# Performance work log

Hardware: AMD Instinct MI355X
Metric: run time of the kernel (lower is better)

Reference implementation:

```python
import jax, jax.numpy as jnp
import numpy as np

N = 50000
E = 800000
IN = 128
HID = 32
OUT = 32
H1, H2 = 4, 4
NEG_SLOPE = 0.2


def setup_inputs() -> dict:
    key = jax.random.key(0)
    ks = jax.random.split(key, 12)
    x = jax.random.normal(ks[0], (N, IN), dtype=jnp.float32)
    src = jax.random.randint(ks[1], (E,), 0, N, dtype=jnp.int32)
    dst = jax.random.randint(ks[2], (E,), 0, N, dtype=jnp.int32)
    s = 0.1
    # layer 1: fc (IN -> H1*HID, no bias), attn vectors (H1, HID), bias (H1*HID,)
    W1 = jax.random.normal(ks[3], (IN, H1 * HID), dtype=jnp.float32) * s
    al1 = jax.random.normal(ks[4], (H1, HID), dtype=jnp.float32) * s
    ar1 = jax.random.normal(ks[5], (H1, HID), dtype=jnp.float32) * s
    b1 = jnp.zeros((H1 * HID,), dtype=jnp.float32)
    # layer 2: fc (H1*HID -> H2*OUT, no bias)
    W2 = jax.random.normal(ks[6], (H1 * HID, H2 * OUT), dtype=jnp.float32) * s
    al2 = jax.random.normal(ks[7], (H2, OUT), dtype=jnp.float32) * s
    ar2 = jax.random.normal(ks[8], (H2, OUT), dtype=jnp.float32) * s
    b2 = jnp.zeros((H2 * OUT,), dtype=jnp.float32)
    return {"x": x, "W1": W1, "al1": al1, "ar1": ar1, "b1": b1,
            "W2": W2, "al2": al2, "ar2": ar2, "b2": b2,
            "src": src, "dst": dst}


def _gat_layer(x, W, al, ar, b, src, dst, n, h, d):
    # feat_drop is identity (eval mode)
    feat = (x @ W).reshape(n, h, d)                       # [N,H,D]
    el = jnp.einsum('nhd,hd->nh', feat, al)               # [N,H]
    er = jnp.einsum('nhd,hd->nh', feat, ar)               # [N,H]
    e = jax.nn.leaky_relu(el[src] + er[dst], NEG_SLOPE)   # [E,H] SDDMM
    # edge softmax over incoming edges of each destination node
    emax = jax.ops.segment_max(e, dst, num_segments=n)    # [N,H]
    emax = jnp.where(jnp.isfinite(emax), emax, 0.0)       # guard 0-in-degree
    w = jnp.exp(e - emax[dst])                            # [E,H]
    denom = jax.ops.segment_sum(w, dst, num_segments=n)   # [N,H]
    alpha = w / jnp.maximum(denom[dst], 1e-9)             # [E,H]; attn_drop identity
    # SpMM aggregation
    rst = jax.ops.segment_sum(feat[src] * alpha[:, :, None], dst, num_segments=n)
    # residual: in_feats == h*d for both layers -> DGL uses Identity res_fc
    rst = rst + x.reshape(n, h, d)
    rst = rst + b.reshape(1, h, d)
    return rst


def reference(x, W1, al1, ar1, b1, W2, al2, ar2, b2, src, dst):
    h = _gat_layer(x, W1, al1, ar1, b1, src, dst, N, H1, HID)
    h = jax.nn.elu(h)                                     # layer-1 activation
    h = h.reshape(N, H1 * HID)                            # flatten(1)
    h = _gat_layer(h, W2, al2, ar2, b2, src, dst, N, H2, OUT)
    return h.mean(axis=1)                                 # [N,OUT]
```

## Files before the change

kernel.cpp:

```cpp
#include <hip/hip_runtime.h>
#include <cstdint>
#include <cstddef>

#define NEG_SLOPE 0.2f

typedef __bf16 bf16x8 __attribute__((ext_vector_type(8)));
typedef float  f32x4  __attribute__((ext_vector_type(4)));

__device__ inline unsigned int bf16pair(float a, float b) {
    unsigned int ua = __float_as_uint(a), ub = __float_as_uint(b);
    ua += 0x7fffu + ((ua >> 16) & 1u);
    ub += 0x7fffu + ((ub >> 16) & 1u);
    return (ua >> 16) | (ub & 0xffff0000u);
}
__device__ inline unsigned short bf16r(float x) {
    unsigned int u = __float_as_uint(x);
    u += 0x7fffu + ((u >> 16) & 1u);
    return (unsigned short)(u >> 16);
}

__global__ __launch_bounds__(256) void wtrans_kernel(
    const float* __restrict__ W1, const float* __restrict__ W2,
    unsigned short* __restrict__ Wt1, unsigned short* __restrict__ Wt2)
{
    __shared__ float tile[64][65];
    const float* W = (blockIdx.x < 4) ? W1 : W2;
    unsigned short* Wt = (blockIdx.x < 4) ? Wt1 : Wt2;
    const int tb = blockIdx.x & 3;
    const int k0 = (tb >> 1) * 64, n0 = (tb & 1) * 64;
    const int c = threadIdx.x & 63, r4 = threadIdx.x >> 6;
#pragma unroll
    for (int i = 0; i < 16; ++i) {
        const int r = i * 4 + r4;
        tile[r][c] = W[(size_t)(k0 + r) * 128 + n0 + c];
    }
    __syncthreads();
#pragma unroll
    for (int i = 0; i < 16; ++i) {
        const int nn = i * 4 + r4;
        Wt[(size_t)(n0 + nn) * 128 + k0 + c] = bf16r(tile[c][nn]);
    }
}

__global__ __launch_bounds__(256, 3) void gemm_attn_kernel(
    const float* __restrict__ X, const unsigned short* __restrict__ Wt,
    const float* __restrict__ al, const float* __restrict__ ar,
    unsigned short* __restrict__ feat16, float* __restrict__ el,
    float* __restrict__ er, int n)
{
    __shared__ unsigned short sX[64][136];
    __shared__ unsigned short sW[128][136];

    const int t = threadIdx.x;
    const int rowbase = blockIdx.x * 64;

#pragma unroll
    for (int i = 0; i < 8; ++i) {
        const int idx = t + 256 * i;
        const int row = idx >> 5;
        const int kq  = (idx & 31) * 4;
        int g = rowbase + row; if (g >= n) g = n - 1;
        const float4 v = *(const float4*)&X[(size_t)g * 128 + kq];
        uint2 pk;
        pk.x = bf16pair(v.x, v.y);
        pk.y = bf16pair(v.z, v.w);
        *(uint2*)&sX[row][kq] = pk;
    }
#pragma unroll
    for (int i = 0; i < 8; ++i) {
        const int idx = t + 256 * i;
        const int row = idx >> 4;
        const int q   = idx & 15;
        *(uint4*)&sW[row][q * 8] = *(const uint4*)&Wt[(size_t)row * 128 + q * 8];
    }
    __syncthreads();

    const int lane = t & 63;
    const int w    = t >> 6;
    const int m    = lane & 15;
    const int g4   = lane >> 4;

    bf16x8 a[4];
#pragma unroll
    for (int ks = 0; ks < 4; ++ks)
        a[ks] = *(const bf16x8*)&sX[w * 16 + m][ks * 32 + g4 * 8];

    float elacc[4][4] = {{0}}, eracc[4][4] = {{0}};
    unsigned short fout[8][4];

#pragma unroll
    for (int ct = 0; ct < 8; ct += 2) {
        f32x4 acc0 = {0.f, 0.f, 0.f, 0.f}, acc1 = {0.f, 0.f, 0.f, 0.f};
        const int n0 = ct * 16 + m, n1 = n0 + 16;
#pragma unroll
        for (int ks = 0; ks < 4; ++ks) {
            const bf16x8 b0 = *(const bf16x8*)&sW[n0][ks * 32 + g4 * 8];
            const bf16x8 b1 = *(const bf16x8*)&sW[n1][ks * 32 + g4 * 8];
            acc0 = __builtin_amdgcn_mfma_f32_16x16x32_bf16(a[ks], b0, acc0, 0, 0, 0);
            acc1 = __builtin_amdgcn_mfma_f32_16x16x32_bf16(a[ks], b1, acc1, 0, 0, 0);
        }
        const int h = ct >> 1;
        const float al0 = al[n0], ar0 = ar[n0];
        const float al1 = al[n1], ar1 = ar[n1];
#pragma unroll
        for (int r = 0; r < 4; ++r) {
            elacc[r][h] += acc0[r] * al0 + acc1[r] * al1;
            eracc[r][h] += acc0[r] * ar0 + acc1[r] * ar1;
            fout[ct][r]     = bf16r(acc0[r]);
            fout[ct + 1][r] = bf16r(acc1[r]);
        }
    }

    __syncthreads();
#pragma unroll
    for (int ct = 0; ct < 8; ++ct)
#pragma unroll
        for (int r = 0; r < 4; ++r)
            sX[w * 16 + g4 * 4 + r][(ct & 1) * 16 + (ct >> 1) * 32 + m] = fout[ct][r];
    __syncthreads();
    {
        const int row = t >> 2;
        const int q   = t & 3;
        const int g   = rowbase + row;
        if (g < n) {
#pragma unroll
            for (int i = 0; i < 4; ++i) {
                const int c0 = q * 8 + i * 32;
                *(uint4*)&feat16[(size_t)g * 128 + c0] = *(const uint4*)&sX[row][c0];
            }
        }
    }

#pragma unroll
    for (int r = 0; r < 4; ++r)
#pragma unroll
        for (int h = 0; h < 4; ++h) {
            float a_ = elacc[r][h], b_ = eracc[r][h];
            a_ += __shfl_xor(a_, 1); b_ += __shfl_xor(b_, 1);
            a_ += __shfl_xor(a_, 2); b_ += __shfl_xor(b_, 2);
            a_ += __shfl_xor(a_, 4); b_ += __shfl_xor(b_, 4);
            a_ += __shfl_xor(a_, 8); b_ += __shfl_xor(b_, 8);
            elacc[r][h] = a_; eracc[r][h] = b_;
        }
    if (m == 0) {
#pragma unroll
        for (int r = 0; r < 4; ++r) {
            const int row = rowbase + w * 16 + g4 * 4 + r;
            if (row < n) {
#pragma unroll
                for (int h = 0; h < 4; ++h) {
                    el[(size_t)row * 4 + h] = elacc[r][h];
                    er[(size_t)row * 4 + h] = eracc[r][h];
                }
            }
        }
    }
}


__global__ void rank_kernel(const int* __restrict__ dst, int* __restrict__ deg,
                            int* __restrict__ rank, int E)
{
    const int e4 = (blockIdx.x * blockDim.x + threadIdx.x) * 4;
    if (e4 + 4 <= E) {
        const int4 d = *(const int4*)&dst[e4];
        int4 r;
        r.x = atomicAdd(&deg[d.x], 1);
        r.y = atomicAdd(&deg[d.y], 1);
        r.z = atomicAdd(&deg[d.z], 1);
        r.w = atomicAdd(&deg[d.w], 1);
        *(int4*)&rank[e4] = r;
    } else {
        for (int e = e4; e < E; ++e) rank[e] = atomicAdd(&deg[dst[e]], 1);
    }
}

__global__ __launch_bounds__(1024) void scan_kernel(
    const int* __restrict__ deg, int* __restrict__ off, int n)
{
    __shared__ int wsums[16];
    __shared__ int s_carry;
    const int tid  = threadIdx.x;
    const int lane = tid & 63;
    const int wid  = tid >> 6;

    if (tid == 0) { s_carry = 0; off[0] = 0; }
    __syncthreads();

    const int n4 = n >> 2;
    const int4* __restrict__ deg4 = (const int4*)deg;

    for (int base = 0; base < n4; base += 1024) {
        const int i4 = base + tid;
        int4 v = make_int4(0, 0, 0, 0);
        if (i4 < n4) v = deg4[i4];
        const int t0 = v.x, t1 = t0 + v.y, t2 = t1 + v.z, t3 = t2 + v.w;

        int x = t3;
#pragma unroll
        for (int d = 1; d < 64; d <<= 1) {
            int y = __shfl_up(x, d);
            if (lane >= d) x += y;
        }
        if (lane == 63) wsums[wid] = x;
        __syncthreads();

        if (wid == 0 && lane < 16) {
            int xx = wsums[lane];
#pragma unroll
            for (int d = 1; d < 16; d <<= 1) {
                int y = __shfl_up(xx, d);
                if (lane >= d) xx += y;
            }
            wsums[lane] = xx;
        }
        __syncthreads();

        const int wp   = (wid == 0) ? 0 : wsums[wid - 1];
        const int excl = s_carry + wp + (x - t3);
        if (i4 < n4) {
            off[4 * i4 + 1] = excl + t0;
            off[4 * i4 + 2] = excl + t1;
            off[4 * i4 + 3] = excl + t2;
            off[4 * i4 + 4] = excl + t3;
        }
        __syncthreads();
        if (tid == 0) s_carry += wsums[15];
        __syncthreads();
    }
}

__global__ void place_kernel(const int* __restrict__ src, const int* __restrict__ dst,
                             const int* __restrict__ off, const int* __restrict__ rank,
                             int* __restrict__ csr_src, int E)
{
    const int e4 = (blockIdx.x * blockDim.x + threadIdx.x) * 4;
    if (e4 + 4 <= E) {
        const int4 s = *(const int4*)&src[e4];
        const int4 d = *(const int4*)&dst[e4];
        const int4 r = *(const int4*)&rank[e4];
        const int o0 = off[d.x], o1 = off[d.y], o2 = off[d.z], o3 = off[d.w];
        csr_src[o0 + r.x] = s.x;
        csr_src[o1 + r.y] = s.y;
        csr_src[o2 + r.z] = s.z;
        csr_src[o3 + r.w] = s.w;
    } else {
        for (int e = e4; e < E; ++e)
            csr_src[off[dst[e]] + rank[e]] = src[e];
    }
}

template <bool LAYER2>
__global__ __launch_bounds__(256) void agg_kernel(
    const int* __restrict__ off, const int* __restrict__ csr_src,
    const unsigned short* __restrict__ feat16, const float* __restrict__ el,
    const float* __restrict__ er, const float* __restrict__ resid,
    const float* __restrict__ bias, float* __restrict__ out, int n)
{
    const int lane = threadIdx.x & 63;
    const int node = blockIdx.x * 4 + (threadIdx.x >> 6);
    if (node >= n) return;

    const int h  = lane >> 4;
    const int d0 = 2 * lane;

    const float erh = er[(size_t)node * 4 + h];
    const unsigned int* __restrict__ fb = (const unsigned int*)feat16;

    const int beg = off[node], end = off[node + 1];

    float acc0 = 0.f, acc1 = 0.f, sw = 0.f;
    int j = beg;

#define EDGE4(J)                                                              \
    {                                                                         \
        const int s0 = csr_src[J], s1 = csr_src[(J) + 1];                     \
        const int s2 = csr_src[(J) + 2], s3 = csr_src[(J) + 3];               \
        const float e0 = el[(size_t)s0 * 4 + h];                              \
        const float e1 = el[(size_t)s1 * 4 + h];                              \
        const float e2 = el[(size_t)s2 * 4 + h];                              \
        const float e3 = el[(size_t)s3 * 4 + h];                              \
        const unsigned int u0 = fb[(size_t)s0 * 64 + lane];                   \
        const unsigned int u1 = fb[(size_t)s1 * 64 + lane];                   \
        const unsigned int u2 = fb[(size_t)s2 * 64 + lane];                   \
        const unsigned int u3 = fb[(size_t)s3 * 64 + lane];                   \
        float a0 = e0 + erh, a1 = e1 + erh, a2 = e2 + erh, a3 = e3 + erh;     \
        a0 = (a0 >= 0.f) ? a0 : NEG_SLOPE * a0;                               \
        a1 = (a1 >= 0.f) ? a1 : NEG_SLOPE * a1;                               \
        a2 = (a2 >= 0.f) ? a2 : NEG_SLOPE * a2;                               \
        a3 = (a3 >= 0.f) ? a3 : NEG_SLOPE * a3;                               \
        const float w0 = __expf(a0), w1 = __expf(a1);                         \
        const float w2 = __expf(a2), w3 = __expf(a3);                         \
        acc0 += w0 * __uint_as_float(u0 << 16);                               \
        acc1 += w0 * __uint_as_float(u0 & 0xffff0000u);                       \
        acc0 += w1 * __uint_as_float(u1 << 16);                               \
        acc1 += w1 * __uint_as_float(u1 & 0xffff0000u);                       \
        acc0 += w2 * __uint_as_float(u2 << 16);                               \
        acc1 += w2 * __uint_as_float(u2 & 0xffff0000u);                       \
        acc0 += w3 * __uint_as_float(u3 << 16);                               \
        acc1 += w3 * __uint_as_float(u3 & 0xffff0000u);                       \
        sw += w0 + w1 + w2 + w3;                                              \
    }

    for (; j + 8 <= end; j += 8) { EDGE4(j) EDGE4(j + 4) }
    for (; j + 4 <= end; j += 4) { EDGE4(j) }
#undef EDGE4
    for (; j < end; ++j) {
        const int s = csr_src[j];
        float e = el[(size_t)s * 4 + h] + erh;
        e = (e >= 0.f) ? e : NEG_SLOPE * e;
        const float w = __expf(e);
        const unsigned int u = fb[(size_t)s * 64 + lane];
        acc0 += w * __uint_as_float(u << 16);
        acc1 += w * __uint_as_float(u & 0xffff0000u);
        sw += w;
    }

    const float inv = 1.f / fmaxf(sw, 1e-9f);
    const float2 rs = *(const float2*)&resid[(size_t)node * 128 + d0];
    float v0 = acc0 * inv + rs.x + bias[d0];
    float v1 = acc1 * inv + rs.y + bias[d0 + 1];

    if (!LAYER2) {
        v0 = (v0 > 0.f) ? v0 : expm1f(v0);
        v1 = (v1 > 0.f) ? v1 : expm1f(v1);
        *(float2*)&out[(size_t)node * 128 + d0] = make_float2(v0, v1);
    } else {
        float s0 = v0, s1 = v1;
        s0 += __shfl_xor(s0, 16); s1 += __shfl_xor(s1, 16);
        s0 += __shfl_xor(s0, 32); s1 += __shfl_xor(s1, 32);
        if (lane < 16)
            *(float2*)&out[(size_t)node * 32 + 2 * lane] =
                make_float2(s0 * 0.25f, s1 * 0.25f);
    }
}

extern "C" void kernel_launch(void* const* d_in, const int* in_sizes, int n_in,
                              void* d_out, int out_size, void* d_ws, size_t ws_size,
                              hipStream_t stream)
{
    const float* x   = (const float*)d_in[0];
    const float* W1  = (const float*)d_in[1];
    const float* al1 = (const float*)d_in[2];
    const float* ar1 = (const float*)d_in[3];
    const float* b1  = (const float*)d_in[4];
    const float* W2  = (const float*)d_in[5];
    const float* al2 = (const float*)d_in[6];
    const float* ar2 = (const float*)d_in[7];
    const float* b2  = (const float*)d_in[8];
    const int*   src = (const int*)d_in[9];
    const int*   dst = (const int*)d_in[10];

    const int n = in_sizes[0] / 128;
    const int E = in_sizes[9];
    float* out = (float*)d_out;

    char* p = (char*)d_ws;
    float* h1    = (float*)p;          p += (size_t)n * 128 * sizeof(float);
    unsigned short* feat16 = (unsigned short*)p; p += (size_t)n * 128 * sizeof(unsigned short);
    float* el    = (float*)p;          p += (size_t)n * 4 * sizeof(float);
    float* er    = (float*)p;          p += (size_t)n * 4 * sizeof(float);
    int* off     = (int*)p;            p += (size_t)(n + 1) * sizeof(int);
    int* deg     = (int*)p;            p += (size_t)n * sizeof(int);
    int* rank    = (int*)p;            p += (size_t)E * sizeof(int);
    int* csr     = (int*)p;            p += (size_t)E * sizeof(int);
    unsigned short* wt1 = (unsigned short*)p; p += (size_t)128 * 128 * sizeof(unsigned short);
    unsigned short* wt2 = (unsigned short*)p; p += (size_t)128 * 128 * sizeof(unsigned short);

    hipMemsetAsync(deg, 0, (size_t)n * sizeof(int), stream);

    const int gemm_grid  = (n + 63) / 64;
    const int edge4_grid = (E / 4 + 255) / 256;
    const int agg_grid   = (n + 3) / 4;

    wtrans_kernel<<<8, 256, 0, stream>>>(W1, W2, wt1, wt2);
    gemm_attn_kernel<<<gemm_grid, 256, 0, stream>>>(x, wt1, al1, ar1, feat16, el, er, n);
    rank_kernel<<<edge4_grid, 256, 0, stream>>>(dst, deg, rank, E);
    scan_kernel<<<1, 1024, 0, stream>>>(deg, off, n);
    place_kernel<<<edge4_grid, 256, 0, stream>>>(src, dst, off, rank, csr, E);
    agg_kernel<false><<<agg_grid, 256, 0, stream>>>(off, csr, feat16, el, er, x, b1, h1, n);
    gemm_attn_kernel<<<gemm_grid, 256, 0, stream>>>(h1, wt2, al2, ar2, feat16, el, er, n);
    agg_kernel<true><<<agg_grid, 256, 0, stream>>>(off, csr, feat16, el, er, h1, b2, out, n);
}
```

Baseline: 271.4 us.

## Split wavefront into two half-waves processing alternate edges with 8-byte feature loads

The aggregation kernel now has each 64-lane wavefront process two edges at once. Each half-wave of 32 lanes covers the full 128-wide bf16 feature row with uint2 loads, and the halves are combined at the end with a cross-lane shuffle. The feature layout written by the projection kernel changes to a plain contiguous column order to match. Attention logits are prescaled by log2(e) so the edge softmax can use the hardware exp2 instruction instead of __expf. The aim is more memory-level parallelism per wave and fewer transcendental ops, at the cost of extra shuffles, half-idle lanes in the epilogue, and a masked tail loop.

Result: no change. 275.9 us (+1.7%).

```diff
diff --git a/kernel.cpp b/kernel.cpp
--- a/kernel.cpp
+++ b/kernel.cpp
@@ -3,6 +3,7 @@
 #include <cstddef>
 
 #define NEG_SLOPE 0.2f
+#define LOG2E 1.44269504088896340736f
 
 typedef __bf16 bf16x8 __attribute__((ext_vector_type(8)));
 typedef float  f32x4  __attribute__((ext_vector_type(4)));
@@ -100,8 +101,8 @@
             acc1 = __builtin_amdgcn_mfma_f32_16x16x32_bf16(a[ks], b1, acc1, 0, 0, 0);
         }
         const int h = ct >> 1;
-        const float al0 = al[n0], ar0 = ar[n0];
-        const float al1 = al[n1], ar1 = ar[n1];
+        const float al0 = al[n0] * LOG2E, ar0 = ar[n0] * LOG2E;
+        const float al1 = al[n1] * LOG2E, ar1 = ar[n1] * LOG2E;
 #pragma unroll
         for (int r = 0; r < 4; ++r) {
             elacc[r][h] += acc0[r] * al0 + acc1[r] * al1;
@@ -116,7 +117,7 @@
     for (int ct = 0; ct < 8; ++ct)
 #pragma unroll
         for (int r = 0; r < 4; ++r)
-            sX[w * 16 + g4 * 4 + r][(ct & 1) * 16 + (ct >> 1) * 32 + m] = fout[ct][r];
+            sX[w * 16 + g4 * 4 + r][ct * 16 + m] = fout[ct][r];
     __syncthreads();
     {
         const int row = t >> 2;
@@ -156,7 +157,6 @@
         }
     }
 }
-
 
 __global__ void rank_kernel(const int* __restrict__ dst, int* __restrict__ deg,
                             int* __restrict__ rank, int E)
@@ -261,77 +261,84 @@
     const int node = blockIdx.x * 4 + (threadIdx.x >> 6);
     if (node >= n) return;
 
-    const int h  = lane >> 4;
-    const int d0 = 2 * lane;
-
-    const float erh = er[(size_t)node * 4 + h];
-    const unsigned int* __restrict__ fb = (const unsigned int*)feat16;
+    const int hh = lane >> 5;
+    const int q  = lane & 31;
+    const int h  = q >> 3;
+
+    const float erh = er[node * 4 + h];
+    const uint2* __restrict__ fb2 = (const uint2*)feat16;
 
     const int beg = off[node], end = off[node + 1];
 
-    float acc0 = 0.f, acc1 = 0.f, sw = 0.f;
+    float a0 = 0.f, a1 = 0.f, a2 = 0.f, a3 = 0.f, sw = 0.f;
+
     int j = beg;
-
-#define EDGE4(J)                                                              \
-    {                                                                         \
-        const int s0 = csr_src[J], s1 = csr_src[(J) + 1];                     \
-        const int s2 = csr_src[(J) + 2], s3 = csr_src[(J) + 3];               \
-        const float e0 = el[(size_t)s0 * 4 + h];                              \
-        const float e1 = el[(size_t)s1 * 4 + h];                              \
-        const float e2 = el[(size_t)s2 * 4 + h];                              \
-        const float e3 = el[(size_t)s3 * 4 + h];                              \
-        const unsigned int u0 = fb[(size_t)s0 * 64 + lane];                   \
-        const unsigned int u1 = fb[(size_t)s1 * 64 + lane];                   \
-        const unsigned int u2 = fb[(size_t)s2 * 64 + lane];                   \
-        const unsigned int u3 = fb[(size_t)s3 * 64 + lane];                   \
-        float a0 = e0 + erh, a1 = e1 + erh, a2 = e2 + erh, a3 = e3 + erh;     \
-        a0 = (a0 >= 0.f) ? a0 : NEG_SLOPE * a0;                               \
-        a1 = (a1 >= 0.f) ? a1 : NEG_SLOPE * a1;                               \
-        a2 = (a2 >= 0.f) ? a2 : NEG_SLOPE * a2;                               \
-        a3 = (a3 >= 0.f) ? a3 : NEG_SLOPE * a3;                               \
-        const float w0 = __expf(a0), w1 = __expf(a1);                         \
-        const float w2 = __expf(a2), w3 = __expf(a3);                         \
-        acc0 += w0 * __uint_as_float(u0 << 16);                               \
-        acc1 += w0 * __uint_as_float(u0 & 0xffff0000u);                       \
-        acc0 += w1 * __uint_as_float(u1 << 16);                               \
-        acc1 += w1 * __uint_as_float(u1 & 0xffff0000u);                       \
-        acc0 += w2 * __uint_as_float(u2 << 16);                               \
-        acc1 += w2 * __uint_as_float(u2 & 0xffff0000u);                       \
-        acc0 += w3 * __uint_as_float(u3 << 16);                               \
-        acc1 += w3 * __uint_as_float(u3 & 0xffff0000u);                       \
-        sw += w0 + w1 + w2 + w3;                                              \
-    }
-
-    for (; j + 8 <= end; j += 8) { EDGE4(j) EDGE4(j + 4) }
-    for (; j + 4 <= end; j += 4) { EDGE4(j) }
-#undef EDGE4
-    for (; j < end; ++j) {
-        const int s = csr_src[j];
-        float e = el[(size_t)s * 4 + h] + erh;
-        e = (e >= 0.f) ? e : NEG_SLOPE * e;
-        const float w = __expf(e);
-        const unsigned int u = fb[(size_t)s * 64 + lane];
-        acc0 += w * __uint_as_float(u << 16);
-        acc1 += w * __uint_as_float(u & 0xffff0000u);
+    for (; j + 4 <= end; j += 4) {
+        const int sA = csr_src[j + hh];
+        const int sB = csr_src[j + 2 + hh];
+        const float eA = el[sA * 4 + h];
+        const float eB = el[sB * 4 + h];
+        const uint2 uA = fb2[sA * 32 + q];
+        const uint2 uB = fb2[sB * 32 + q];
+        float tA = eA + erh; tA = fmaxf(tA, NEG_SLOPE * tA);
+        float tB = eB + erh; tB = fmaxf(tB, NEG_SLOPE * tB);
+        const float wA = __builtin_amdgcn_exp2f(tA);
+        const float wB = __builtin_amdgcn_exp2f(tB);
+        a0 += wA * __uint_as_float(uA.x << 16);
+        a1 += wA * __uint_as_float(uA.x & 0xffff0000u);
+        a2 += wA * __uint_as_float(uA.y << 16);
+        a3 += wA * __uint_as_float(uA.y & 0xffff0000u);
+        a0 += wB * __uint_as_float(uB.x << 16);
+        a1 += wB * __uint_as_float(uB.x & 0xffff0000u);
+        a2 += wB * __uint_as_float(uB.y << 16);
+        a3 += wB * __uint_as_float(uB.y & 0xffff0000u);
+        sw += wA + wB;
+    }
+    for (; j < end; j += 2) {
+        const int jj = j + hh;
+        const bool vld = jj < end;
+        const int s = csr_src[vld ? jj : j];
+        const float e = el[s * 4 + h];
+        const uint2 u = fb2[s * 32 + q];
+        float t = e + erh; t = fmaxf(t, NEG_SLOPE * t);
+        const float w = vld ? __builtin_amdgcn_exp2f(t) : 0.f;
+        a0 += w * __uint_as_float(u.x << 16);
+        a1 += w * __uint_as_float(u.x & 0xffff0000u);
+        a2 += w * __uint_as_float(u.y << 16);
+        a3 += w * __uint_as_float(u.y & 0xffff0000u);
         sw += w;
     }
 
+    a0 += __shfl_xor(a0, 32);
+    a1 += __shfl_xor(a1, 32);
+    a2 += __shfl_xor(a2, 32);
+    a3 += __shfl_xor(a3, 32);
+    sw += __shfl_xor(sw, 32);
+
     const float inv = 1.f / fmaxf(sw, 1e-9f);
-    const float2 rs = *(const float2*)&resid[(size_t)node * 128 + d0];
-    float v0 = acc0 * inv + rs.x + bias[d0];
-    float v1 = acc1 * inv + rs.y + bias[d0 + 1];
+    const float4 rs = *(const float4*)&resid[node * 128 + q * 4];
+    const float4 bs = *(const float4*)&bias[q * 4];
+    float v0 = a0 * inv + rs.x + bs.x;
+    float v1 = a1 * inv + rs.y + bs.y;
+    float v2 = a2 * inv + rs.z + bs.z;
+    float v3 = a3 * inv + rs.w + bs.w;
 
     if (!LAYER2) {
-        v0 = (v0 > 0.f) ? v0 : expm1f(v0);
-        v1 = (v1 > 0.f) ? v1 : expm1f(v1);
-        *(float2*)&out[(size_t)node * 128 + d0] = make_float2(v0, v1);
+        if (lane < 32) {
+            v0 = (v0 > 0.f) ? v0 : expm1f(v0);
+            v1 = (v1 > 0.f) ? v1 : expm1f(v1);
+            v2 = (v2 > 0.f) ? v2 : expm1f(v2);
+            v3 = (v3 > 0.f) ? v3 : expm1f(v3);
+            *(float4*)&out[node * 128 + q * 4] = make_float4(v0, v1, v2, v3);
+        }
     } else {
-        float s0 = v0, s1 = v1;
-        s0 += __shfl_xor(s0, 16); s1 += __shfl_xor(s1, 16);
-        s0 += __shfl_xor(s0, 32); s1 += __shfl_xor(s1, 32);
-        if (lane < 16)
-            *(float2*)&out[(size_t)node * 32 + 2 * lane] =
-                make_float2(s0 * 0.25f, s1 * 0.25f);
+        v0 += __shfl_xor(v0, 8);  v1 += __shfl_xor(v1, 8);
+        v2 += __shfl_xor(v2, 8);  v3 += __shfl_xor(v3, 8);
+        v0 += __shfl_xor(v0, 16); v1 += __shfl_xor(v1, 16);
+        v2 += __shfl_xor(v2, 16); v3 += __shfl_xor(v3, 16);
+        if (lane < 8)
+            *(float4*)&out[node * 32 + q * 4] =
+                make_float4(v0 * 0.25f, v1 * 0.25f, v2 * 0.25f, v3 * 0.25f);
     }
 }
 
```
